# Optimization experiments

Measured on AMD Instinct MI355X. Metric: run time of the kernel, lower is better.

The kernel has to match this reference:

```python
import jax, jax.numpy as jnp
import numpy as np

V, D, E, S, L = 32000, 1024, 2048, 128, 4  # vocab, d_model, e=expansion*d, d_head, n_layers
B, T = 2, 2048


def _layernorm(x, g, b, eps=1e-5):
    mu = jnp.mean(x, axis=-1, keepdims=True)
    var = jnp.var(x, axis=-1, keepdims=True)
    return (x - mu) * jax.lax.rsqrt(var + eps) * g + b


def _rope_tables(t, dim):
    half = dim // 2
    inv_freq = 1.0 / (10000.0 ** (jnp.arange(0, dim, 2, dtype=jnp.float32) / dim))  # (half,)
    freqs = jnp.arange(t, dtype=jnp.float32)[:, None] * inv_freq[None, :]           # (T, half)
    return jnp.cos(freqs), jnp.sin(freqs)


def _apply_rope(x, cos, sin):
    half = x.shape[-1] // 2
    x1, x2 = x[..., :half], x[..., half:]
    return jnp.concatenate([x1 * cos - x2 * sin, x1 * sin + x2 * cos], axis=-1)


def setup_inputs() -> dict:
    key = jax.random.key(0)
    ks = jax.random.split(key, 12)
    def init(k, shape, fan_in):
        return jax.random.normal(k, shape, jnp.float32) * (fan_in ** -0.5)
    return {
        "tokens": jax.random.randint(ks[0], (B, T), 0, V, dtype=jnp.int64),
        "emb":    init(ks[1], (V, D), D),
        "Wu":     init(ks[2], (L, D, E), D),
        "Wv":     init(ks[3], (L, D, E), D),
        "Wq":     init(ks[4], (L, E, S), E),
        "Wk":     init(ks[5], (L, E, S), E),
        "Wo":     init(ks[6], (L, E, D), E),
        "ln_g":   jnp.ones((L, D), jnp.float32),
        "ln_b":   jnp.zeros((L, D), jnp.float32),
        "lnf_g":  jnp.ones((D,), jnp.float32),
        "lnf_b":  jnp.zeros((D,), jnp.float32),
        "Wlm":    init(ks[7], (D, V), D),
    }


def reference(tokens, emb, Wu, Wv, Wq, Wk, Wo, ln_g, ln_b, lnf_g, lnf_b, Wlm):
    t = tokens.shape[1]
    cos, sin = _rope_tables(t, S)                      # (T, S/2) each
    causal = jnp.tril(jnp.ones((t, t), bool))          # causal mask
    scale = 1.0 / np.sqrt(S)
    x = emb[tokens]                                    # (B, T, D)
    for i in range(L):
        xn = _layernorm(x, ln_g[i], ln_b[i])
        u = jax.nn.silu(xn @ Wu[i])                    # (B, T, E) gate branch
        v = jax.nn.silu(xn @ Wv[i])                    # (B, T, E) value branch
        q = _apply_rope(u @ Wq[i], cos, sin)           # (B, T, S)
        k = _apply_rope(v @ Wk[i], cos, sin)           # (B, T, S)
        attn = jnp.einsum('bts,bus->btu', q, k) * scale   # (B, T, T) single-head
        attn = jnp.where(causal, attn, -1e9)
        attn = jnp.square(jnp.maximum(attn, 0.0))      # relu^2 instead of softmax
        av = jnp.einsum('btu,bue->bte', attn, v)       # (B, T, E)
        x = x + (u * av) @ Wo[i]                       # gated output + residual
    x = _layernorm(x, lnf_g, lnf_b)
    return x @ Wlm                                     # (B, T, V) logits
```

## Files before the change

kernel.cpp:

```cpp
#include <hip/hip_runtime.h>
#include <math.h>


#define Bz 2
#define Tt 2048
#define Dd 1024
#define Ee 2048
#define Ss 128
#define Ll 4
#define Vv 32000
#define BT (Bz * Tt)

typedef __attribute__((ext_vector_type(8))) _Float16 f16x8;
typedef __attribute__((ext_vector_type(4))) _Float16 f16x4;
typedef __attribute__((ext_vector_type(4))) float    f32x4;

__device__ __forceinline__ void load_lds16(const void* g, void* l) {
  __builtin_amdgcn_global_load_lds(
      (const __attribute__((address_space(1))) void*)g,
      (__attribute__((address_space(3))) void*)l, 16, 0, 0);
}

#define BM 128
#define BN 128
#define BK 32

enum { EPI_F32 = 0, EPI_SILU = 1, EPI_SCORES = 2, EPI_RESID = 3 };

template <int EPI>
__global__ void __launch_bounds__(256, 2) gemm_bt(
    const _Float16* __restrict__ A, long sA,
    const _Float16* __restrict__ Bt, long sB,
    void* __restrict__ Cp, long sC,
    int M, int N, int K, int lda, int ldb, int ldc, int causal) {
  int bm = blockIdx.x, bn = blockIdx.y, bz = blockIdx.z;
  if (EPI == EPI_SCORES && bn > bm) return;
  A += (size_t)bz * sA;
  Bt += (size_t)bz * sB;

  int Keff = K;
  if (causal == 2) {
    int km = (bm + 1) * BM;
    Keff = km < K ? km : K;
  }

  __shared__ __align__(16) _Float16 As[BM * BK];
  __shared__ __align__(16) _Float16 Bs[BN * BK];

  int tid = threadIdx.x;
  int lane = tid & 63, wave = tid >> 6;
  int wr = (wave >> 1) << 6;
  int wc = (wave & 1) << 6;
  int row0 = bm * BM, col0 = bn * BN;
  int fr = lane & 15;
  int kg = lane >> 4;
  int srow = lane >> 2;
  int scol = (lane & 3) << 3;

  f32x4 acc[4][4];
#pragma unroll
  for (int i = 0; i < 4; i++)
#pragma unroll
    for (int j = 0; j < 4; j++)
#pragma unroll
      for (int e = 0; e < 4; e++) acc[i][j][e] = 0.f;

  const f16x8* As8 = (const f16x8*)As;
  const f16x8* Bs8 = (const f16x8*)Bs;

  for (int k0 = 0; k0 < Keff; k0 += BK) {
    __syncthreads();
#pragma unroll
    for (int i = 0; i < 2; i++) {
      int rb = (wave * 2 + i) * 16;
      load_lds16(A + (size_t)(row0 + rb + srow) * lda + k0 + scol,
                 (void*)&As[rb * BK]);
      load_lds16(Bt + (size_t)(col0 + rb + srow) * ldb + k0 + scol,
                 (void*)&Bs[rb * BK]);
    }
    asm volatile("s_waitcnt vmcnt(0)" ::: "memory");
    __syncthreads();

    f16x8 af[4], bf[4];
#pragma unroll
    for (int m = 0; m < 4; m++)
      af[m] = As8[(size_t)(wr + m * 16 + fr) * (BK / 8) + kg];
#pragma unroll
    for (int n = 0; n < 4; n++)
      bf[n] = Bs8[(size_t)(wc + n * 16 + fr) * (BK / 8) + kg];
#pragma unroll
    for (int m = 0; m < 4; m++)
#pragma unroll
      for (int n = 0; n < 4; n++)
        acc[m][n] =
            __builtin_amdgcn_mfma_f32_16x16x32_f16(af[m], bf[n], acc[m][n], 0, 0, 0);
  }

#pragma unroll
  for (int m = 0; m < 4; m++) {
    int gr0 = row0 + wr + m * 16 + (kg << 2);
#pragma unroll
    for (int n = 0; n < 4; n++) {
      int gc = col0 + wc + n * 16 + fr;
#pragma unroll
      for (int r = 0; r < 4; r++) {
        float v = acc[m][n][r];
        size_t ci = (size_t)(gr0 + r) * ldc + gc;
        if (EPI == EPI_F32) {
          ((float*)Cp + (size_t)bz * sC)[ci] = v;
        } else if (EPI == EPI_SILU) {
          ((_Float16*)Cp + (size_t)bz * sC)[ci] =
              (_Float16)(v / (1.f + expf(-v)));
        } else if (EPI == EPI_SCORES) {
          float s = v * 0.08838834764831845f;
          s = fmaxf(s, 0.f);
          s = (gc <= gr0 + r) ? s * s : 0.f;
          ((_Float16*)Cp + (size_t)bz * sC)[ci] = (_Float16)s;
        } else {
          ((float*)Cp)[ci] += v;
        }
      }
    }
  }
}

__global__ void __launch_bounds__(256) ln_kernel(const float* __restrict__ x,
                                                 const float* __restrict__ g,
                                                 const float* __restrict__ b,
                                                 _Float16* __restrict__ out) {
  int row = blockIdx.x, tid = threadIdx.x;
  float4 v = ((const float4*)(x + (size_t)row * Dd))[tid];
  float s = v.x + v.y + v.z + v.w;
  float q = v.x * v.x + v.y * v.y + v.z * v.z + v.w * v.w;
#pragma unroll
  for (int off = 32; off > 0; off >>= 1) {
    s += __shfl_down(s, off, 64);
    q += __shfl_down(q, off, 64);
  }
  __shared__ float ss[4], sq[4];
  int lane = tid & 63, wv = tid >> 6;
  if (lane == 0) { ss[wv] = s; sq[wv] = q; }
  __syncthreads();
  s = ss[0] + ss[1] + ss[2] + ss[3];
  q = sq[0] + sq[1] + sq[2] + sq[3];
  float mu = s * (1.f / Dd);
  float var = q * (1.f / Dd) - mu * mu;
  float rs = rsqrtf(var + 1e-5f);
  float4 gg = ((const float4*)g)[tid];
  float4 bb = ((const float4*)b)[tid];
  f16x4 o;
  o[0] = (_Float16)((v.x - mu) * rs * gg.x + bb.x);
  o[1] = (_Float16)((v.y - mu) * rs * gg.y + bb.y);
  o[2] = (_Float16)((v.z - mu) * rs * gg.z + bb.z);
  o[3] = (_Float16)((v.w - mu) * rs * gg.w + bb.w);
  ((f16x4*)(out + (size_t)row * Dd))[tid] = o;
}

__global__ void embed_kernel(const int* __restrict__ toks,
                             const float* __restrict__ emb,
                             float* __restrict__ x) {
  int row = blockIdx.x, tid = threadIdx.x;
  long t = toks[row];
  ((float4*)(x + (size_t)row * Dd))[tid] =
      ((const float4*)(emb + (size_t)t * Dd))[tid];
}

__global__ void rope_table_kernel(float* __restrict__ cosT,
                                  float* __restrict__ sinT) {
  int idx = blockIdx.x * 256 + threadIdx.x;
  int t = idx >> 6, i = idx & 63;
  float inv = powf(10000.f, (float)(2 * i) * (-1.f / 128.f));
  float a = (float)t * inv;
  cosT[idx] = cosf(a);
  sinT[idx] = sinf(a);
}

__global__ void rope_kernel(const float* __restrict__ pre,
                            _Float16* __restrict__ o16,
                            const float* __restrict__ cosT,
                            const float* __restrict__ sinT) {
  int row = blockIdx.x * 4 + threadIdx.y;
  int i = threadIdx.x;
  int z = blockIdx.y;
  const float* p = pre + (size_t)z * BT * Ss + (size_t)row * Ss;
  _Float16* o = o16 + (size_t)z * BT * Ss + (size_t)row * Ss;
  int t = row & (Tt - 1);
  float c = cosT[t * 64 + i], sn = sinT[t * 64 + i];
  float x1 = p[i], x2 = p[i + 64];
  o[i] = (_Float16)(x1 * c - x2 * sn);
  o[i + 64] = (_Float16)(x1 * sn + x2 * c);
}

__global__ void gated_kernel(const _Float16* __restrict__ u,
                             const float* __restrict__ av,
                             _Float16* __restrict__ g) {
  size_t i = ((size_t)blockIdx.x * 256 + threadIdx.x) * 4;
  f16x4 uu = *(const f16x4*)(u + i);
  float4 aa = *(const float4*)(av + i);
  f16x4 o;
  o[0] = (_Float16)((float)uu[0] * aa.x);
  o[1] = (_Float16)((float)uu[1] * aa.y);
  o[2] = (_Float16)((float)uu[2] * aa.z);
  o[3] = (_Float16)((float)uu[3] * aa.w);
  *(f16x4*)(g + i) = o;
}

template <typename TIn>
__global__ void transconv_kernel(const TIn* __restrict__ in,
                                 _Float16* __restrict__ out, int R, int C,
                                 long s_in, long s_out) {
  __shared__ float tile[64][65];
  in += (size_t)blockIdx.z * s_in;
  out += (size_t)blockIdx.z * s_out;
  int r0 = blockIdx.y * 64, c0 = blockIdx.x * 64;
  int tx = threadIdx.x & 63, ty = threadIdx.x >> 6;
#pragma unroll
  for (int p = 0; p < 16; p++) {
    int r = p * 4 + ty;
    tile[r][tx] = (float)in[(size_t)(r0 + r) * C + c0 + tx];
  }
  __syncthreads();
#pragma unroll
  for (int p = 0; p < 16; p++) {
    int r = p * 4 + ty;
    out[(size_t)(c0 + r) * R + r0 + tx] = (_Float16)tile[tx][r];
  }
}

extern "C" void kernel_launch(void* const* d_in, const int* in_sizes, int n_in,
                              void* d_out, int out_size, void* d_ws,
                              size_t ws_size, hipStream_t stream) {
  const int*   tokens = (const int*)d_in[0];
  const float* emb    = (const float*)d_in[1];
  const float* Wu     = (const float*)d_in[2];
  const float* Wv     = (const float*)d_in[3];
  const float* Wq     = (const float*)d_in[4];
  const float* Wk     = (const float*)d_in[5];
  const float* Wo     = (const float*)d_in[6];
  const float* ln_g   = (const float*)d_in[7];
  const float* ln_b   = (const float*)d_in[8];
  const float* lnf_g  = (const float*)d_in[9];
  const float* lnf_b  = (const float*)d_in[10];
  const float* Wlm    = (const float*)d_in[11];
  float* out = (float*)d_out;
  (void)in_sizes; (void)n_in; (void)out_size;

  char* wsp = (char*)d_ws;
  size_t off = 0;
  auto alloc = [&](size_t bytes) -> void* {
    void* p = wsp + off;
    off = (off + bytes + 255) & ~(size_t)255;
    return p;
  };

  float*    x     = (float*)alloc((size_t)BT * Dd * 4);
  _Float16* xn    = (_Float16*)alloc((size_t)BT * Dd * 2);
  _Float16* uvh   = (_Float16*)alloc((size_t)2 * BT * Ee * 2);
  _Float16* vT    = (_Float16*)alloc((size_t)Bz * Ee * Tt * 2);
  float*    qkpre = (float*)alloc((size_t)2 * BT * Ss * 4);
  _Float16* qkh   = (_Float16*)alloc((size_t)2 * BT * Ss * 2);
  _Float16* attn  = (_Float16*)alloc((size_t)Bz * Tt * Tt * 2);
  float*    av    = (float*)alloc((size_t)BT * Ee * 4);
  _Float16* gh    = (_Float16*)alloc((size_t)BT * Ee * 2);
  float*    cosT  = (float*)alloc((size_t)Tt * 64 * 4);
  float*    sinT  = (float*)alloc((size_t)Tt * 64 * 4);
  _Float16* WuvT  = (_Float16*)alloc((size_t)2 * Ll * Ee * Dd * 2);
  _Float16* WqkT  = (_Float16*)alloc((size_t)2 * Ll * Ss * Ee * 2);
  _Float16* WoT   = (_Float16*)alloc((size_t)Ll * Dd * Ee * 2);
  _Float16* WlmT  = (_Float16*)alloc((size_t)Vv * Dd * 2);
  if (off > ws_size) return;

  transconv_kernel<float><<<dim3(Ee / 64, Dd / 64, Ll), 256, 0, stream>>>(
      Wu, WuvT, Dd, Ee, (long)Dd * Ee, (long)Ee * Dd);
  transconv_kernel<float><<<dim3(Ee / 64, Dd / 64, Ll), 256, 0, stream>>>(
      Wv, WuvT + (size_t)Ll * Ee * Dd, Dd, Ee, (long)Dd * Ee, (long)Ee * Dd);
  transconv_kernel<float><<<dim3(Ss / 64, Ee / 64, Ll), 256, 0, stream>>>(
      Wq, WqkT, Ee, Ss, (long)Ee * Ss, (long)Ss * Ee);
  transconv_kernel<float><<<dim3(Ss / 64, Ee / 64, Ll), 256, 0, stream>>>(
      Wk, WqkT + (size_t)Ll * Ss * Ee, Ee, Ss, (long)Ee * Ss, (long)Ss * Ee);
  transconv_kernel<float><<<dim3(Dd / 64, Ee / 64, Ll), 256, 0, stream>>>(
      Wo, WoT, Ee, Dd, (long)Ee * Dd, (long)Dd * Ee);
  transconv_kernel<float><<<dim3(Vv / 64, Dd / 64, 1), 256, 0, stream>>>(
      Wlm, WlmT, Dd, Vv, 0, 0);

  rope_table_kernel<<<(Tt * 64) / 256, 256, 0, stream>>>(cosT, sinT);
  embed_kernel<<<BT, 256, 0, stream>>>(tokens, emb, x);

  for (int l = 0; l < Ll; l++) {
    ln_kernel<<<BT, 256, 0, stream>>>(x, ln_g + (size_t)l * Dd,
                                      ln_b + (size_t)l * Dd, xn);
    gemm_bt<EPI_SILU><<<dim3(BT / BM, Ee / BN, 2), 256, 0, stream>>>(
        xn, 0, WuvT + (size_t)l * Ee * Dd, (long)Ll * Ee * Dd, (void*)uvh,
        (long)BT * Ee, BT, Ee, Dd, Dd, Dd, Ee, 0);
    gemm_bt<EPI_F32><<<dim3(BT / BM, Ss / BN, 2), 256, 0, stream>>>(
        uvh, (long)BT * Ee, WqkT + (size_t)l * Ss * Ee, (long)Ll * Ss * Ee,
        (void*)qkpre, (long)BT * Ss, BT, Ss, Ee, Ee, Ee, Ss, 0);
    rope_kernel<<<dim3(BT / 4, 2), dim3(64, 4), 0, stream>>>(qkpre, qkh, cosT,
                                                             sinT);
    transconv_kernel<_Float16><<<dim3(Ee / 64, Tt / 64, Bz), 256, 0, stream>>>(
        uvh + (size_t)BT * Ee, vT, Tt, Ee, (long)Tt * Ee, (long)Ee * Tt);
    gemm_bt<EPI_SCORES><<<dim3(Tt / BM, Tt / BN, Bz), 256, 0, stream>>>(
        qkh, (long)Tt * Ss, qkh + (size_t)BT * Ss, (long)Tt * Ss, (void*)attn,
        (long)Tt * Tt, Tt, Tt, Ss, Ss, Ss, Tt, 0);
    gemm_bt<EPI_F32><<<dim3(Tt / BM, Ee / BN, Bz), 256, 0, stream>>>(
        attn, (long)Tt * Tt, vT, (long)Ee * Tt, (void*)av, (long)Tt * Ee, Tt,
        Ee, Tt, Tt, Tt, Ee, 2);
    gated_kernel<<<(BT * Ee / 4) / 256, 256, 0, stream>>>(uvh, av, gh);
    gemm_bt<EPI_RESID><<<dim3(BT / BM, Dd / BN, 1), 256, 0, stream>>>(
        gh, 0, WoT + (size_t)l * Dd * Ee, 0, (void*)x, 0, BT, Dd, Ee, Ee, Ee,
        Dd, 0);
  }

  ln_kernel<<<BT, 256, 0, stream>>>(x, lnf_g, lnf_b, xn);
  gemm_bt<EPI_F32><<<dim3(BT / BM, Vv / BN, 1), 256, 0, stream>>>(
      xn, 0, WlmT, 0, (void*)out, 0, BT, Vv, Dd, Dd, Dd, Vv, 0);
}
```

Before: 1.430 ms.

## Add 256x256 pipelined GEMM for big projections and fuse gating into AV GEMM

Adds a new 512-thread GEMM kernel with 256x256 tiles, K=64 double-buffered LDS loads, swizzled LDS layout, XCD-aware block remapping and setprio-interleaved MFMA phases. It is used for the Wu/Wv projection and the LM head. Separately, the u*av gating is fused into the attention-value GEMM epilogue, which drops the fp32 av buffer and the standalone gated kernel. The new kernel uses 128KB of LDS and a large accumulator register footprint, and the fused epilogue does scalar fp16 loads of u.

```diff
diff --git a/kernel.cpp b/kernel.cpp
--- a/kernel.cpp
+++ b/kernel.cpp
@@ -21,18 +21,149 @@
       (__attribute__((address_space(3))) void*)l, 16, 0, 0);
 }
 
+#define FENCE asm volatile("" ::: "memory")
+#define BARRIER do { FENCE; __builtin_amdgcn_s_barrier(); FENCE; } while (0)
+#define LGKM0 do { asm volatile("s_waitcnt lgkmcnt(0)" ::: "memory"); \
+                   __builtin_amdgcn_sched_barrier(0); } while (0)
+
+enum { EPI_F32 = 0, EPI_SILU = 1, EPI_SCORES = 2, EPI_RESID = 3, EPI_GATED = 4 };
+
+__device__ __forceinline__ int xcd_swz(int id, int nwg) {
+  int q = nwg >> 3, r = nwg & 7;
+  int x = id & 7, o = id >> 3;
+  return (x < r ? x * (q + 1) : r * (q + 1) + (x - r) * q) + o;
+}
+
+template <int EPI>
+__global__ void __launch_bounds__(512) gemm256(
+    const _Float16* __restrict__ A, long sA,
+    const _Float16* __restrict__ Bt, long sB,
+    void* __restrict__ Cp, long sC,
+    int M, int N, int K, int lda, int ldb, int ldc) {
+  const int bz = blockIdx.z;
+  A += (size_t)bz * sA;
+  Bt += (size_t)bz * sB;
+
+  const int nbm = M >> 8;
+  const int id = xcd_swz(blockIdx.x, gridDim.x);
+  const int bm = id % nbm, bn = id / nbm;
+  const int row0 = bm << 8, col0 = bn << 8;
+
+  __shared__ __align__(16) _Float16 Abuf[2][256 * 64];
+  __shared__ __align__(16) _Float16 Bbuf[2][256 * 64];
+
+  const int tid = threadIdx.x, lane = tid & 63, w = tid >> 6;
+  const int mu = w >> 2, nu = w & 3;
+  const int fr = lane & 15, kg = lane >> 4;
+  const int srow = (w << 3) + (lane >> 3);
+  const int sg = (lane & 7) ^ ((lane >> 3) & 7);
+  const _Float16* Asrc = A + (size_t)(row0 + srow) * lda + sg * 8;
+  const _Float16* Bsrc = Bt + (size_t)(col0 + srow) * ldb + sg * 8;
+  const int gx[2] = { ((kg) ^ (fr & 7)) << 3, ((4 + kg) ^ (fr & 7)) << 3 };
+
+#define ST_A(BUF, KT, Q) load_lds16(Asrc + (size_t)(Q) * 64 * lda + (size_t)(KT) * 64, \
+                                    (void*)&Abuf[BUF][(Q) * 4096 + (w << 9)])
+#define ST_B(BUF, KT, Q) load_lds16(Bsrc + (size_t)(Q) * 64 * ldb + (size_t)(KT) * 64, \
+                                    (void*)&Bbuf[BUF][(Q) * 4096 + (w << 9)])
+#define RD_A(BUF, MH)                                                          \
+  { _Pragma("unroll") for (int j = 0; j < 4; ++j)                              \
+    _Pragma("unroll") for (int ks = 0; ks < 2; ++ks)                           \
+      af[j][ks] = *(const f16x8*)&Abuf[BUF][(mu * 128 + (MH) * 64 + j * 16 + fr) * 64 + gx[ks]]; }
+#define RD_B(BUF, NH, BQ)                                                      \
+  { _Pragma("unroll") for (int i = 0; i < 2; ++i)                              \
+    _Pragma("unroll") for (int ks = 0; ks < 2; ++ks)                           \
+      BQ[i][ks] = *(const f16x8*)&Bbuf[BUF][(nu * 64 + (NH) * 32 + i * 16 + fr) * 64 + gx[ks]]; }
+#define MFMA_Q(MH, NH, BQ)                                                     \
+  { _Pragma("unroll") for (int j = 0; j < 4; ++j)                              \
+    _Pragma("unroll") for (int i = 0; i < 2; ++i)                              \
+    _Pragma("unroll") for (int ks = 0; ks < 2; ++ks)                           \
+      acc[(MH) * 4 + j][(NH) * 2 + i] = __builtin_amdgcn_mfma_f32_16x16x32_f16( \
+          af[j][ks], BQ[i][ks], acc[(MH) * 4 + j][(NH) * 2 + i], 0, 0, 0); }
+
+  f32x4 acc[8][4];
+#pragma unroll
+  for (int m = 0; m < 8; ++m)
+#pragma unroll
+    for (int n = 0; n < 4; ++n)
+#pragma unroll
+      for (int e = 0; e < 4; ++e) acc[m][n][e] = 0.f;
+
+  f16x8 af[4][2], bfA[2][2], bfB[2][2];
+
+  const int NT = K >> 6;
+  ST_B(0, 0, 0); ST_B(0, 0, 1); ST_B(0, 0, 2); ST_B(0, 0, 3);
+  ST_A(0, 0, 0); ST_A(0, 0, 2); ST_A(0, 0, 1); ST_A(0, 0, 3);
+  asm volatile("s_waitcnt vmcnt(2)" ::: "memory");
+  BARRIER;
+
+  for (int t = 0; t < NT; ++t) {
+    const int b = t & 1, nb = b ^ 1;
+    const int kn = (t + 1 < NT) ? t + 1 : t;
+    RD_A(b, 0);
+    RD_B(b, 0, bfA);
+    ST_B(nb, kn, 0); ST_B(nb, kn, 1);
+    BARRIER;
+    LGKM0;
+    __builtin_amdgcn_s_setprio(1); MFMA_Q(0, 0, bfA); __builtin_amdgcn_s_setprio(0);
+    BARRIER;
+    RD_B(b, 1, bfB);
+    ST_B(nb, kn, 2); ST_B(nb, kn, 3);
+    BARRIER;
+    LGKM0;
+    __builtin_amdgcn_s_setprio(1); MFMA_Q(0, 1, bfB); __builtin_amdgcn_s_setprio(0);
+    asm volatile("s_waitcnt vmcnt(4)" ::: "memory");
+    BARRIER;
+    RD_A(b, 1);
+    ST_A(nb, kn, 0); ST_A(nb, kn, 2);
+    BARRIER;
+    LGKM0;
+    __builtin_amdgcn_s_setprio(1); MFMA_Q(1, 0, bfA); __builtin_amdgcn_s_setprio(0);
+    BARRIER;
+    ST_A(nb, kn, 1); ST_A(nb, kn, 3);
+    BARRIER;
+    LGKM0;
+    __builtin_amdgcn_s_setprio(1); MFMA_Q(1, 1, bfB); __builtin_amdgcn_s_setprio(0);
+    asm volatile("s_waitcnt vmcnt(2)" ::: "memory");
+    BARRIER;
+  }
+  asm volatile("s_waitcnt vmcnt(0)" ::: "memory");
+
+#pragma unroll
+  for (int m = 0; m < 8; ++m) {
+    int gr0 = row0 + mu * 128 + m * 16 + (kg << 2);
+#pragma unroll
+    for (int n = 0; n < 4; ++n) {
+      int gc = col0 + nu * 64 + n * 16 + fr;
+#pragma unroll
+      for (int r = 0; r < 4; ++r) {
+        float v = acc[m][n][r];
+        size_t ci = (size_t)(gr0 + r) * ldc + gc;
+        if (EPI == EPI_F32) {
+          ((float*)Cp + (size_t)bz * sC)[ci] = v;
+        } else {
+          ((_Float16*)Cp + (size_t)bz * sC)[ci] = (_Float16)(v / (1.f + expf(-v)));
+        }
+      }
+    }
+  }
+#undef ST_A
+#undef ST_B
+#undef RD_A
+#undef RD_B
+#undef MFMA_Q
+}
+
 #define BM 128
 #define BN 128
 #define BK 32
-
-enum { EPI_F32 = 0, EPI_SILU = 1, EPI_SCORES = 2, EPI_RESID = 3 };
 
 template <int EPI>
 __global__ void __launch_bounds__(256, 2) gemm_bt(
     const _Float16* __restrict__ A, long sA,
     const _Float16* __restrict__ Bt, long sB,
     void* __restrict__ Cp, long sC,
-    int M, int N, int K, int lda, int ldb, int ldc, int causal) {
+    int M, int N, int K, int lda, int ldb, int ldc, int causal,
+    const _Float16* __restrict__ U) {
   int bm = blockIdx.x, bn = blockIdx.y, bz = blockIdx.z;
   if (EPI == EPI_SCORES && bn > bm) return;
   A += (size_t)bz * sA;
@@ -116,6 +247,9 @@
           s = fmaxf(s, 0.f);
           s = (gc <= gr0 + r) ? s * s : 0.f;
           ((_Float16*)Cp + (size_t)bz * sC)[ci] = (_Float16)s;
+        } else if (EPI == EPI_GATED) {
+          const _Float16* Ub = U + (size_t)bz * sC;
+          ((_Float16*)Cp + (size_t)bz * sC)[ci] = (_Float16)((float)Ub[ci] * v);
         } else {
           ((float*)Cp)[ci] += v;
         }
@@ -191,20 +325,6 @@
   o[i + 64] = (_Float16)(x1 * sn + x2 * c);
 }
 
-__global__ void gated_kernel(const _Float16* __restrict__ u,
-                             const float* __restrict__ av,
-                             _Float16* __restrict__ g) {
-  size_t i = ((size_t)blockIdx.x * 256 + threadIdx.x) * 4;
-  f16x4 uu = *(const f16x4*)(u + i);
-  float4 aa = *(const float4*)(av + i);
-  f16x4 o;
-  o[0] = (_Float16)((float)uu[0] * aa.x);
-  o[1] = (_Float16)((float)uu[1] * aa.y);
-  o[2] = (_Float16)((float)uu[2] * aa.z);
-  o[3] = (_Float16)((float)uu[3] * aa.w);
-  *(f16x4*)(g + i) = o;
-}
-
 template <typename TIn>
 __global__ void transconv_kernel(const TIn* __restrict__ in,
                                  _Float16* __restrict__ out, int R, int C,
@@ -260,7 +380,6 @@
   float*    qkpre = (float*)alloc((size_t)2 * BT * Ss * 4);
   _Float16* qkh   = (_Float16*)alloc((size_t)2 * BT * Ss * 2);
   _Float16* attn  = (_Float16*)alloc((size_t)Bz * Tt * Tt * 2);
-  float*    av    = (float*)alloc((size_t)BT * Ee * 4);
   _Float16* gh    = (_Float16*)alloc((size_t)BT * Ee * 2);
   float*    cosT  = (float*)alloc((size_t)Tt * 64 * 4);
   float*    sinT  = (float*)alloc((size_t)Tt * 64 * 4);
@@ -289,29 +408,28 @@
   for (int l = 0; l < Ll; l++) {
     ln_kernel<<<BT, 256, 0, stream>>>(x, ln_g + (size_t)l * Dd,
                                       ln_b + (size_t)l * Dd, xn);
-    gemm_bt<EPI_SILU><<<dim3(BT / BM, Ee / BN, 2), 256, 0, stream>>>(
+    gemm256<EPI_SILU><<<dim3((BT / 256) * (Ee / 256), 1, 2), 512, 0, stream>>>(
         xn, 0, WuvT + (size_t)l * Ee * Dd, (long)Ll * Ee * Dd, (void*)uvh,
-        (long)BT * Ee, BT, Ee, Dd, Dd, Dd, Ee, 0);
+        (long)BT * Ee, BT, Ee, Dd, Dd, Dd, Ee);
     gemm_bt<EPI_F32><<<dim3(BT / BM, Ss / BN, 2), 256, 0, stream>>>(
         uvh, (long)BT * Ee, WqkT + (size_t)l * Ss * Ee, (long)Ll * Ss * Ee,
-        (void*)qkpre, (long)BT * Ss, BT, Ss, Ee, Ee, Ee, Ss, 0);
+        (void*)qkpre, (long)BT * Ss, BT, Ss, Ee, Ee, Ee, Ss, 0, nullptr);
     rope_kernel<<<dim3(BT / 4, 2), dim3(64, 4), 0, stream>>>(qkpre, qkh, cosT,
                                                              sinT);
     transconv_kernel<_Float16><<<dim3(Ee / 64, Tt / 64, Bz), 256, 0, stream>>>(
         uvh + (size_t)BT * Ee, vT, Tt, Ee, (long)Tt * Ee, (long)Ee * Tt);
     gemm_bt<EPI_SCORES><<<dim3(Tt / BM, Tt / BN, Bz), 256, 0, stream>>>(
         qkh, (long)Tt * Ss, qkh + (size_t)BT * Ss, (long)Tt * Ss, (void*)attn,
-        (long)Tt * Tt, Tt, Tt, Ss, Ss, Ss, Tt, 0);
-    gemm_bt<EPI_F32><<<dim3(Tt / BM, Ee / BN, Bz), 256, 0, stream>>>(
-        attn, (long)Tt * Tt, vT, (long)Ee * Tt, (void*)av, (long)Tt * Ee, Tt,
-        Ee, Tt, Tt, Tt, Ee, 2);
-    gated_kernel<<<(BT * Ee / 4) / 256, 256, 0, stream>>>(uvh, av, gh);
+        (long)Tt * Tt, Tt, Tt, Ss, Ss, Ss, Tt, 0, nullptr);
+    gemm_bt<EPI_GATED><<<dim3(Tt / BM, Ee / BN, Bz), 256, 0, stream>>>(
+        attn, (long)Tt * Tt, vT, (long)Ee * Tt, (void*)gh, (long)Tt * Ee, Tt,
+        Ee, Tt, Tt, Tt, Ee, 2, uvh);
     gemm_bt<EPI_RESID><<<dim3(BT / BM, Dd / BN, 1), 256, 0, stream>>>(
         gh, 0, WoT + (size_t)l * Dd * Ee, 0, (void*)x, 0, BT, Dd, Ee, Ee, Ee,
-        Dd, 0);
+        Dd, 0, nullptr);
   }
 
   ln_kernel<<<BT, 256, 0, stream>>>(x, lnf_g, lnf_b, xn);
-  gemm_bt<EPI_F32><<<dim3(BT / BM, Vv / BN, 1), 256, 0, stream>>>(
-      xn, 0, WlmT, 0, (void*)out, 0, BT, Vv, Dd, Dd, Dd, Vv, 0);
-}
+  gemm256<EPI_F32><<<dim3((BT / 256) * (Vv / 256), 1, 1), 512, 0, stream>>>(
+      xn, 0, WlmT, 0, (void*)out, 0, BT, Vv, Dd, Dd, Dd, Vv);
+}
```

Measured after the change: 1.389 ms. -2.8%, faster.
